# Kernel tuning notes

Hardware: AMD Instinct MI355X
Metric: run time of the kernel (lower is better)

The kernel has to match this reference:

```python
import jax, jax.numpy as jnp
import numpy as np

H = 8          # num_attention_heads
HEAD_DIM = 24  # 192 / 8


def setup_inputs() -> dict:
    key = jax.random.key(0)
    k1, k2, k3 = jax.random.split(key, 3)
    B, S, D = 4, 2048, 192
    x = jax.random.normal(k1, (B, S, D), dtype=jnp.float32)
    mask0 = jnp.zeros((B, 1, 1, S), dtype=jnp.float32)  # HF additive attention mask
    w_attn = jax.random.normal(k2, (D, 3 * D), dtype=jnp.float32) * 0.02
    b_attn = jnp.zeros((3 * D,), dtype=jnp.float32)
    w_proj = jax.random.normal(k3, (D, D), dtype=jnp.float32) * 0.02
    b_proj = jnp.zeros((D,), dtype=jnp.float32)
    return {"x": x, "mask0": mask0, "w_attn": w_attn, "b_attn": b_attn,
            "w_proj": w_proj, "b_proj": b_proj}


def reference(x, mask0, w_attn, b_attn, w_proj, b_proj):
    B, S, D = x.shape
    # fused QKV projection (GPT2 Conv1D: x @ W + b)
    qkv = x @ w_attn + b_attn                       # [B,S,3D]
    q, k, v = jnp.split(qkv, 3, axis=-1)
    def split_heads(t):
        return t.reshape(B, S, H, HEAD_DIM).transpose(0, 2, 1, 3)  # [B,H,S,hd]
    q, k, v = split_heads(q), split_heads(k), split_heads(v)
    # scaled QK^T
    scores = jnp.einsum('bhqd,bhkd->bhqk', q, k) / jnp.sqrt(
        jnp.asarray(HEAD_DIM, dtype=q.dtype))
    # causal mask (masked_fill with dtype min), then additive padding mask
    causal = jnp.tril(jnp.ones((S, S), dtype=bool))
    mask_value = jnp.finfo(scores.dtype).min
    scores = jnp.where(causal, scores, mask_value) + mask0
    attn = jax.nn.softmax(scores, axis=-1)          # [B,H,S,S]
    # attn_dropout is identity in eval mode
    out = jnp.einsum('bhqk,bhkd->bhqd', attn, v)    # [B,H,S,hd]
    out = out.transpose(0, 2, 1, 3).reshape(B, S, D)
    return out @ w_proj + b_proj
```

## Files before the change

kernel.cpp:

```cpp
#include <hip/hip_runtime.h>

typedef unsigned short u16;
typedef unsigned int u32;
typedef __bf16 bf16x8 __attribute__((ext_vector_type(8)));
typedef float f32x4 __attribute__((ext_vector_type(4)));
typedef float f32x16 __attribute__((ext_vector_type(16)));
typedef u32 u32x2 __attribute__((ext_vector_type(2)));
typedef u32 u32x4 __attribute__((ext_vector_type(4)));

#define NB 4
#define NS 2048
#define ND 192
#define NH 8
#define HD 24
#define NM (NB*NS)
#define N3 (3*ND)
#define NBH (NB*NH)
#define NROWS (NBH*NS)
#define NPART 2

#define LOG2E 1.4426950408889634f
#define QSCALE (0.20412414523193152f * 1.4426950408889634f)

__device__ __forceinline__ u16 f2bf(float f){
  union { float f; unsigned u; } a; a.f = f;
  unsigned r = a.u + 0x7fffu + ((a.u >> 16) & 1u);
  return (u16)(r >> 16);
}
__device__ __forceinline__ float b2f(u16 h){
  union { u32 u; float f; } a; a.u = ((u32)h) << 16; return a.f;
}
__device__ __forceinline__ u32 cvtpk(float lo, float hi){
  u32 r; asm("v_cvt_pk_bf16_f32 %0, %1, %2" : "=v"(r) : "v"(lo), "v"(hi)); return r;
}
__device__ __forceinline__ void pswap(u32 &a, u32 &b){
  asm("v_permlane32_swap_b32 %0, %1" : "+v"(a), "+v"(b));
}

__device__ __forceinline__ void transpose64(
    const float* __restrict__ src, int srcN, u16* __restrict__ dst, int dstK,
    int k0, int n0, u16 (*sh)[68], int tid)
{
  int r = tid >> 2, cs = tid & 3;
  const float* sp = src + (size_t)(k0 + r)*srcN + n0 + cs*16;
  #pragma unroll
  for (int q = 0; q < 4; ++q) {
    float4 v = *(const float4*)(sp + q*4);
    u16 o[4] = { f2bf(v.x), f2bf(v.y), f2bf(v.z), f2bf(v.w) };
    *(u32x2*)&sh[r][cs*16 + q*4] = *(const u32x2*)o;
  }
  __syncthreads();
  int n = tid >> 2, ks = tid & 3;
  u16 tmp[16];
  #pragma unroll
  for (int j = 0; j < 16; ++j) tmp[j] = sh[ks*16 + j][n];
  u16* dp = dst + (size_t)(n0 + n)*dstK + k0 + ks*16;
  *(u32x4*)dp       = *(const u32x4*)tmp;
  *(u32x4*)(dp + 8) = *(const u32x4*)(tmp + 8);
}

__global__ __launch_bounds__(256) void prep_kernel(
    const float* __restrict__ w_attn, const float* __restrict__ w_proj,
    u16* __restrict__ wta, u16* __restrict__ wtp)
{
  __shared__ u16 sh[64][68];
  const int bid = blockIdx.x, tid = threadIdx.x;
  if (bid < 27) {
    int kt = bid/9, nt = bid%9;
    transpose64(w_attn, N3, wta, ND, kt*64, nt*64, sh, tid);
  } else {
    int t = bid - 27; int kt = t/3, nt = t%3;
    transpose64(w_proj, ND, wtp, ND, kt*64, nt*64, sh, tid);
  }
}

__global__ __launch_bounds__(256) void qkv_kernel(
    const float* __restrict__ x, const u16* __restrict__ wta,
    const float* __restrict__ b_attn, const float* __restrict__ mask0,
    u16* __restrict__ qp, u16* __restrict__ kp, u16* __restrict__ vtp)
{
  __shared__ u16 tile[96*72];
  const int m0 = blockIdx.x*64, n0 = blockIdx.y*96;
  const int tid = threadIdx.x;
  const int w = tid >> 6, lane = tid & 63, c = lane & 15, g = lane >> 4;
  f32x4 acc[6] = {};
  const int ar = m0 + w*16 + c;
  const float* xrow = x + (size_t)ar*ND;
  #pragma unroll
  for (int ks = 0; ks < 6; ++ks) {
    float4 xa = *(const float4*)(xrow + ks*32 + g*8);
    float4 xc = *(const float4*)(xrow + ks*32 + g*8 + 4);
    union { u32 wrd[4]; bf16x8 v; } afu;
    afu.wrd[0] = cvtpk(xa.x, xa.y); afu.wrd[1] = cvtpk(xa.z, xa.w);
    afu.wrd[2] = cvtpk(xc.x, xc.y); afu.wrd[3] = cvtpk(xc.z, xc.w);
    bf16x8 af = afu.v;
    #pragma unroll
    for (int t = 0; t < 6; ++t) {
      bf16x8 bfr = *(const bf16x8*)(wta + (size_t)(n0 + t*16 + c)*ND + ks*32 + g*8);
      acc[t] = __builtin_amdgcn_mfma_f32_16x16x32_bf16(af, bfr, acc[t], 0, 0, 0);
    }
  }
  const int b = m0 >> 11, sb = m0 & (NS-1);
  if (n0 >= 384) {
    const int h0 = (n0 - 384)/HD;
    #pragma unroll
    for (int t = 0; t < 6; ++t) {
      float bias = b_attn[n0 + t*16 + c];
      #pragma unroll
      for (int r = 0; r < 4; ++r)
        tile[(t*16 + c)*72 + w*16 + g*4 + r] = f2bf(acc[t][r] + bias);
    }
    __syncthreads();
    const int chunk = tid & 7;
    u16 ones[8] = {0x3F80,0x3F80,0x3F80,0x3F80,0x3F80,0x3F80,0x3F80,0x3F80};
    #pragma unroll
    for (int rr = 0; rr < 4; ++rr) {
      int row = rr*32 + (tid >> 3);
      if (row < 96) {
        int hl = row/HD, dv = row - hl*HD;
        u16* dst = vtp + ((size_t)((b*NH + h0 + hl)*32 + dv))*NS + sb + chunk*8;
        *(u32x4*)dst = *(const u32x4*)&tile[row*72 + chunk*8];
      } else if (row < 100) {
        int hl = row - 96;
        u16* dst = vtp + ((size_t)((b*NH + h0 + hl)*32 + 24))*NS + sb + chunk*8;
        *(u32x4*)dst = *(const u32x4*)ones;
      }
    }
  } else {
    const bool isQ = (n0 < 192);
    const float scl = isQ ? QSCALE : 1.0f;
    #pragma unroll
    for (int t = 0; t < 6; ++t) {
      float bias = b_attn[n0 + t*16 + c];
      #pragma unroll
      for (int r = 0; r < 4; ++r)
        tile[(w*16 + g*4 + r)*104 + t*16 + c] = f2bf((acc[t][r] + bias)*scl);
    }
    __syncthreads();
    int row = tid >> 2, run = tid & 3;
    int h0 = (n0 % 192)/HD;
    u16 d24 = isQ ? (u16)0x3F80
                  : f2bf(mask0[b*NS + sb + row] * LOG2E);
    const u16* src = &tile[row*104 + run*24];
    union { u32x4 q[4]; u16 s[32]; } buf;
    buf.q[0] = *(const u32x4*)(src);
    buf.q[1] = *(const u32x4*)(src + 8);
    buf.q[2] = *(const u32x4*)(src + 16);
    buf.s[24] = d24;
    #pragma unroll
    for (int j = 25; j < 32; ++j) buf.s[j] = 0;
    u16* dst = (isQ ? qp : kp)
             + ((size_t)((b*NH + h0 + run)*NS) + sb + row)*32;
    #pragma unroll
    for (int q = 0; q < 4; ++q)
      *(u32x4*)(dst + q*8) = buf.q[q];
  }
}

__global__ __launch_bounds__(256) void attn_kernel(
    const u16* __restrict__ qp, const u16* __restrict__ kp,
    const u16* __restrict__ vtp, u16* __restrict__ po, float* __restrict__ pmf)
{
  __shared__ u16 klds[2][64][40];
  __shared__ u16 vlds[2][32][72];

  const int bh = blockIdx.x;
  const int g  = 15 - (int)blockIdx.y;
  const int part = blockIdx.z;
  const int tid = threadIdx.x;
  const int w = tid >> 6, lane = tid & 63, c = lane & 31, hi = lane >> 5;
  const int q0 = g*128 + w*32;
  const int cnt = g + 1;
  const int t0 = part*cnt;

  const size_t qkbase = (size_t)bh*NS*32;

  const u16* qrow = qp + qkbase + (size_t)(q0 + c)*32;
  bf16x8 qf0 = *(const bf16x8*)(qrow + hi*8);
  bf16x8 qf1 = *(const bf16x8*)(qrow + 16 + hi*8);

  const int krow = tid >> 2, kch = tid & 3;
  const int vrow = tid >> 3, vch = tid & 7;
  const u16* kgsrc = kp + qkbase + (size_t)(t0*64 + krow)*32 + kch*8;
  const u16* vgsrc = vtp + ((size_t)(bh*32 + vrow))*NS + t0*64 + vch*8;

  f32x16 o = {0};
  const f32x16 z16 = {0};
  float m = 0.f;

  u32x4 kreg = *(const u32x4*)(kgsrc);
  u32x4 vreg = *(const u32x4*)(vgsrc);
  *(u32x4*)&klds[0][krow][kch*8] = kreg;
  *(u32x4*)&vlds[0][vrow][vch*8] = vreg;
  __syncthreads();

  for (int dt = 0; dt < cnt; ++dt) {
    const int cur = dt & 1;
    if (dt + 1 < cnt) {
      kreg = *(const u32x4*)(kgsrc + (size_t)(dt+1)*64*32);
      vreg = *(const u32x4*)(vgsrc + (dt+1)*64);
    }
    const int kb0 = (t0 + dt)*64;
    if (kb0 <= q0) {
      const bool a1 = (kb0 + 32 <= q0);
      bf16x8 ka0 = *(const bf16x8*)&klds[cur][c][hi*8];
      bf16x8 ka1 = *(const bf16x8*)&klds[cur][c][16 + hi*8];
      __builtin_amdgcn_s_setprio(1);
      f32x16 st = __builtin_amdgcn_mfma_f32_32x32x16_bf16(ka0, qf0, z16, 0, 0, 0);
      st        = __builtin_amdgcn_mfma_f32_32x32x16_bf16(ka1, qf1, st,  0, 0, 0);
      __builtin_amdgcn_s_setprio(0);
      f32x16 su;
      if (a1) {
        bf16x8 kb0f = *(const bf16x8*)&klds[cur][32 + c][hi*8];
        bf16x8 kb1f = *(const bf16x8*)&klds[cur][32 + c][16 + hi*8];
        __builtin_amdgcn_s_setprio(1);
        su = __builtin_amdgcn_mfma_f32_32x32x16_bf16(kb0f, qf0, z16, 0, 0, 0);
        su = __builtin_amdgcn_mfma_f32_32x32x16_bf16(kb1f, qf1, su,  0, 0, 0);
        __builtin_amdgcn_s_setprio(0);
      }
      float pm = -3.0e38f;
      if (kb0 == q0) {
        #pragma unroll
        for (int r = 0; r < 16; ++r) {
          int krel = (r & 3) + 8*(r >> 2) + 4*hi;
          float s = (krel > c) ? -3.0e38f : st[r];
          st[r] = s; pm = fmaxf(pm, s);
        }
      } else {
        #pragma unroll
        for (int r = 0; r < 16; ++r) pm = fmaxf(pm, st[r]);
      }
      if (a1) {
        if (kb0 + 32 == q0) {
          #pragma unroll
          for (int r = 0; r < 16; ++r) {
            int krel = (r & 3) + 8*(r >> 2) + 4*hi;
            float s = (krel > c) ? -3.0e38f : su[r];
            su[r] = s; pm = fmaxf(pm, s);
          }
        } else {
          #pragma unroll
          for (int r = 0; r < 16; ++r) pm = fmaxf(pm, su[r]);
        }
      }
      if (!__all(pm - m <= 8.f)) {
        float pm2 = fmaxf(pm, __shfl_xor(pm, 32));
        float mn = fmaxf(m, pm2);
        float al = __builtin_amdgcn_exp2f(m - mn);
        #pragma unroll
        for (int r = 0; r < 16; ++r) o[r] *= al;
        m = mn;
      }
      #pragma unroll
      for (int r = 0; r < 16; ++r) st[r] = __builtin_amdgcn_exp2f(st[r] - m);
      if (a1) {
        #pragma unroll
        for (int r = 0; r < 16; ++r) su[r] = __builtin_amdgcn_exp2f(su[r] - m);
      }
      {
        u32 a0 = cvtpk(st[0], st[1]),  b0 = cvtpk(st[4], st[5]);
        u32 a1w = cvtpk(st[2], st[3]), b1 = cvtpk(st[6], st[7]);
        pswap(a0, b0); pswap(a1w, b1);
        u32 a2 = cvtpk(st[8], st[9]),  b2 = cvtpk(st[12], st[13]);
        u32 a3 = cvtpk(st[10], st[11]), b3 = cvtpk(st[14], st[15]);
        pswap(a2, b2); pswap(a3, b3);
        union { u32 wrd[4]; bf16x8 v; } pf0, pf1;
        pf0.wrd[0] = a0; pf0.wrd[1] = a1w; pf0.wrd[2] = b0; pf0.wrd[3] = b1;
        pf1.wrd[0] = a2; pf1.wrd[1] = a3;  pf1.wrd[2] = b2; pf1.wrd[3] = b3;
        bf16x8 va0 = *(const bf16x8*)&vlds[cur][c][hi*8];
        bf16x8 va1 = *(const bf16x8*)&vlds[cur][c][16 + hi*8];
        __builtin_amdgcn_s_setprio(1);
        o = __builtin_amdgcn_mfma_f32_32x32x16_bf16(va0, pf0.v, o, 0, 0, 0);
        o = __builtin_amdgcn_mfma_f32_32x32x16_bf16(va1, pf1.v, o, 0, 0, 0);
        __builtin_amdgcn_s_setprio(0);
      }
      if (a1) {
        u32 a0 = cvtpk(su[0], su[1]),  b0 = cvtpk(su[4], su[5]);
        u32 a1w = cvtpk(su[2], su[3]), b1 = cvtpk(su[6], su[7]);
        pswap(a0, b0); pswap(a1w, b1);
        u32 a2 = cvtpk(su[8], su[9]),  b2 = cvtpk(su[12], su[13]);
        u32 a3 = cvtpk(su[10], su[11]), b3 = cvtpk(su[14], su[15]);
        pswap(a2, b2); pswap(a3, b3);
        union { u32 wrd[4]; bf16x8 v; } pf0, pf1;
        pf0.wrd[0] = a0; pf0.wrd[1] = a1w; pf0.wrd[2] = b0; pf0.wrd[3] = b1;
        pf1.wrd[0] = a2; pf1.wrd[1] = a3;  pf1.wrd[2] = b2; pf1.wrd[3] = b3;
        bf16x8 va0 = *(const bf16x8*)&vlds[cur][c][32 + hi*8];
        bf16x8 va1 = *(const bf16x8*)&vlds[cur][c][48 + hi*8];
        __builtin_amdgcn_s_setprio(1);
        o = __builtin_amdgcn_mfma_f32_32x32x16_bf16(va0, pf0.v, o, 0, 0, 0);
        o = __builtin_amdgcn_mfma_f32_32x32x16_bf16(va1, pf1.v, o, 0, 0, 0);
        __builtin_amdgcn_s_setprio(0);
      }
    }
    if (dt + 1 < cnt) {
      *(u32x4*)&klds[cur^1][krow][kch*8] = kreg;
      *(u32x4*)&vlds[cur^1][vrow][vch*8] = vreg;
    }
    __syncthreads();
  }

  const int pidx = part*NROWS + bh*NS + q0 + c;
  u16* porow = po + (size_t)pidx*32;
  #pragma unroll
  for (int rr = 0; rr < 4; ++rr) {
    u32 lo = cvtpk(o[rr*4 + 0], o[rr*4 + 1]);
    u32 h2 = cvtpk(o[rr*4 + 2], o[rr*4 + 3]);
    u32x2 wv = {lo, h2};
    *(u32x2*)(porow + rr*8 + hi*4) = wv;
  }
  if (hi == 0) pmf[pidx] = (t0*64 <= q0) ? m : -3.0e38f;
}

__global__ __launch_bounds__(256) void proj_kernel(
    const u16* __restrict__ po, const float* __restrict__ pmf,
    const u16* __restrict__ wtp, const float* __restrict__ bp,
    float* __restrict__ out)
{
  const int m0 = blockIdx.x*64, n0 = blockIdx.y*64;
  const int tid = threadIdx.x;
  const int w = tid >> 6, lane = tid & 63, c = lane & 15, g = lane >> 4;
  const int ar = m0 + w*16 + c;
  const int b = ar >> 11, s = ar & (NS-1);

  bf16x8 af[6];
  #pragma unroll
  for (int ks = 0; ks < 6; ++ks) {
    int ch = ks*32 + g*8;
    int h = ch / HD, dd = ch - h*HD;
    size_t ridx = (size_t)(b*NH + h)*NS + s;
    float m1 = pmf[ridx], m2 = pmf[NROWS + ridx];
    float M = fmaxf(m1, m2);
    float w1 = __builtin_amdgcn_exp2f(m1 - M);
    float w2 = __builtin_amdgcn_exp2f(m2 - M);
    const u16* r1 = po + ridx*32;
    const u16* r2 = po + ((size_t)NROWS + ridx)*32;
    u32x4 pa = *(const u32x4*)(r1 + dd);
    u32x4 pb = *(const u32x4*)(r2 + dd);
    float l = b2f(r1[24])*w1 + b2f(r2[24])*w2;
    float inv = 1.0f / l;
    float s1 = w1*inv, s2 = w2*inv;
    union { u32 wrd[4]; bf16x8 v; } fu;
    #pragma unroll
    for (int jj = 0; jj < 4; ++jj) {
      u32 wa = pa[jj], wb = pb[jj];
      float v0 = b2f((u16)(wa & 0xffff))*s1 + b2f((u16)(wb & 0xffff))*s2;
      float v1 = b2f((u16)(wa >> 16))*s1 + b2f((u16)(wb >> 16))*s2;
      fu.wrd[jj] = cvtpk(v0, v1);
    }
    af[ks] = fu.v;
  }

  f32x4 acc[4] = {};
  #pragma unroll
  for (int ks = 0; ks < 6; ++ks) {
    #pragma unroll
    for (int t = 0; t < 4; ++t) {
      bf16x8 bfr = *(const bf16x8*)(wtp + (size_t)(n0 + t*16 + c)*ND + ks*32 + g*8);
      acc[t] = __builtin_amdgcn_mfma_f32_16x16x32_bf16(af[ks], bfr, acc[t], 0, 0, 0);
    }
  }
  #pragma unroll
  for (int t = 0; t < 4; ++t) {
    int n = n0 + t*16 + c;
    float bias = bp[n];
    #pragma unroll
    for (int r = 0; r < 4; ++r) {
      int mm = m0 + w*16 + g*4 + r;
      out[(size_t)mm*ND + n] = acc[t][r] + bias;
    }
  }
}

extern "C" void kernel_launch(void* const* d_in, const int* in_sizes, int n_in,
                              void* d_out, int out_size, void* d_ws, size_t ws_size,
                              hipStream_t stream)
{
  const float* x      = (const float*)d_in[0];
  const float* mask0  = (const float*)d_in[1];
  const float* w_attn = (const float*)d_in[2];
  const float* b_attn = (const float*)d_in[3];
  const float* w_proj = (const float*)d_in[4];
  const float* b_proj = (const float*)d_in[5];
  float* out = (float*)d_out;

  char* ws = (char*)d_ws;
  u16*   qp  = (u16*)(ws);
  u16*   kp  = (u16*)(ws + ((size_t)4  << 20));
  u16*   vtp = (u16*)(ws + ((size_t)8  << 20));
  u16*   wta = (u16*)(ws + ((size_t)12 << 20));
  u16*   wtp = (u16*)(ws + ((size_t)12 << 20) + 256*1024);
  u16*   po  = (u16*)(ws + ((size_t)13 << 20));
  float* pmf = (float*)(ws + ((size_t)21 << 20));

  prep_kernel<<<36, 256, 0, stream>>>(w_attn, w_proj, wta, wtp);
  qkv_kernel<<<dim3(NM/64, 6), 256, 0, stream>>>(x, wta, b_attn, mask0,
                                                 qp, kp, vtp);
  attn_kernel<<<dim3(NBH, 16, NPART), 256, 0, stream>>>(qp, kp, vtp, po, pmf);
  proj_kernel<<<dim3(NM/64, ND/64), 256, 0, stream>>>(po, pmf, wtp, b_proj, out);
}
```

Measured before the change: 130.4 us.

## Split causal attention into fixed-size KV chunks with variable partial merge

Measured after the change: 151.1 us. 15.8% more time.

```diff
diff --git a/kernel.cpp b/kernel.cpp
--- a/kernel.cpp
+++ b/kernel.cpp
@@ -17,7 +17,8 @@
 #define N3 (3*ND)
 #define NBH (NB*NH)
 #define NROWS (NBH*NS)
-#define NPART 2
+#define NCHUNK 72
+#define MAXPART 8
 
 #define LOG2E 1.4426950408889634f
 #define QSCALE (0.20412414523193152f * 1.4426950408889634f)
@@ -164,14 +165,20 @@
   __shared__ u16 klds[2][64][40];
   __shared__ u16 vlds[2][32][72];
 
-  const int bh = blockIdx.x;
-  const int g  = 15 - (int)blockIdx.y;
-  const int part = blockIdx.z;
+  const int chunk = blockIdx.x;
+  const int bh = blockIdx.y;
+  int t = (int)sqrtf((float)chunk + 0.5f);
+  while (t*t > chunk) --t;
+  while ((t+1)*(t+1) <= chunk) ++t;
+  const int g = (chunk < t*t + t) ? (2*t - 1) : (2*t);
+  const int cumg = (g & 1) ? (((g-1)/2 + 1)*((g-1)/2 + 1)) : ((g/2)*(g/2) + g/2);
+  const int part = chunk - cumg;
+  const int t0 = part*4;
+  const int cnt = min(4, 2*g + 2 - t0);
+
   const int tid = threadIdx.x;
   const int w = tid >> 6, lane = tid & 63, c = lane & 31, hi = lane >> 5;
   const int q0 = g*128 + w*32;
-  const int cnt = g + 1;
-  const int t0 = part*cnt;
 
   const size_t qkbase = (size_t)bh*NS*32;
 
@@ -318,36 +325,38 @@
 {
   const int m0 = blockIdx.x*64, n0 = blockIdx.y*64;
   const int tid = threadIdx.x;
-  const int w = tid >> 6, lane = tid & 63, c = lane & 15, g = lane >> 4;
+  const int w = tid >> 6, lane = tid & 63, c = lane & 15, gl = lane >> 4;
   const int ar = m0 + w*16 + c;
   const int b = ar >> 11, s = ar & (NS-1);
+  const int np = ((s >> 7) + 2) >> 1;
 
   bf16x8 af[6];
   #pragma unroll
   for (int ks = 0; ks < 6; ++ks) {
-    int ch = ks*32 + g*8;
+    int ch = ks*32 + gl*8;
     int h = ch / HD, dd = ch - h*HD;
     size_t ridx = (size_t)(b*NH + h)*NS + s;
-    float m1 = pmf[ridx], m2 = pmf[NROWS + ridx];
-    float M = fmaxf(m1, m2);
-    float w1 = __builtin_amdgcn_exp2f(m1 - M);
-    float w2 = __builtin_amdgcn_exp2f(m2 - M);
-    const u16* r1 = po + ridx*32;
-    const u16* r2 = po + ((size_t)NROWS + ridx)*32;
-    u32x4 pa = *(const u32x4*)(r1 + dd);
-    u32x4 pb = *(const u32x4*)(r2 + dd);
-    float l = b2f(r1[24])*w1 + b2f(r2[24])*w2;
+    float M = -3.0e38f;
+    for (int p = 0; p < np; ++p) M = fmaxf(M, pmf[(size_t)p*NROWS + ridx]);
+    float v[8] = {}; float l = 0.f;
+    for (int p = 0; p < np; ++p) {
+      float wp = __builtin_amdgcn_exp2f(pmf[(size_t)p*NROWS + ridx] - M);
+      const u16* rp = po + ((size_t)p*NROWS + ridx)*32;
+      u32x4 pa = *(const u32x4*)(rp + dd);
+      l += b2f(rp[24])*wp;
+      #pragma unroll
+      for (int jj = 0; jj < 4; ++jj) {
+        u32 wa = pa[jj];
+        v[jj*2]   += b2f((u16)(wa & 0xffff))*wp;
+        v[jj*2+1] += b2f((u16)(wa >> 16))*wp;
+      }
+    }
     float inv = 1.0f / l;
-    float s1 = w1*inv, s2 = w2*inv;
-    union { u32 wrd[4]; bf16x8 v; } fu;
-    #pragma unroll
-    for (int jj = 0; jj < 4; ++jj) {
-      u32 wa = pa[jj], wb = pb[jj];
-      float v0 = b2f((u16)(wa & 0xffff))*s1 + b2f((u16)(wb & 0xffff))*s2;
-      float v1 = b2f((u16)(wa >> 16))*s1 + b2f((u16)(wb >> 16))*s2;
-      fu.wrd[jj] = cvtpk(v0, v1);
-    }
-    af[ks] = fu.v;
+    union { u32 wrd[4]; bf16x8 vv; } fu;
+    #pragma unroll
+    for (int jj = 0; jj < 4; ++jj)
+      fu.wrd[jj] = cvtpk(v[jj*2]*inv, v[jj*2+1]*inv);
+    af[ks] = fu.vv;
   }
 
   f32x4 acc[4] = {};
@@ -355,7 +364,7 @@
   for (int ks = 0; ks < 6; ++ks) {
     #pragma unroll
     for (int t = 0; t < 4; ++t) {
-      bf16x8 bfr = *(const bf16x8*)(wtp + (size_t)(n0 + t*16 + c)*ND + ks*32 + g*8);
+      bf16x8 bfr = *(const bf16x8*)(wtp + (size_t)(n0 + t*16 + c)*ND + ks*32 + gl*8);
       acc[t] = __builtin_amdgcn_mfma_f32_16x16x32_bf16(af[ks], bfr, acc[t], 0, 0, 0);
     }
   }
@@ -365,7 +374,7 @@
     float bias = bp[n];
     #pragma unroll
     for (int r = 0; r < 4; ++r) {
-      int mm = m0 + w*16 + g*4 + r;
+      int mm = m0 + w*16 + gl*4 + r;
       out[(size_t)mm*ND + n] = acc[t][r] + bias;
     }
   }
@@ -390,11 +399,11 @@
   u16*   wta = (u16*)(ws + ((size_t)12 << 20));
   u16*   wtp = (u16*)(ws + ((size_t)12 << 20) + 256*1024);
   u16*   po  = (u16*)(ws + ((size_t)13 << 20));
-  float* pmf = (float*)(ws + ((size_t)21 << 20));
+  float* pmf = (float*)(ws + ((size_t)45 << 20));
 
   prep_kernel<<<36, 256, 0, stream>>>(w_attn, w_proj, wta, wtp);
   qkv_kernel<<<dim3(NM/64, 6), 256, 0, stream>>>(x, wta, b_attn, mask0,
                                                  qp, kp, vtp);
-  attn_kernel<<<dim3(NBH, 16, NPART), 256, 0, stream>>>(qp, kp, vtp, po, pmf);
+  attn_kernel<<<dim3(NCHUNK, NBH), 256, 0, stream>>>(qp, kp, vtp, po, pmf);
   proj_kernel<<<dim3(NM/64, ND/64), 256, 0, stream>>>(po, pmf, wtp, b_proj, out);
 }
```
